# Kernel optimization log

Measured on AMD Instinct MI355X. Metric: run time of the kernel, lower is better.

## Reference

```python
import jax, jax.numpy as jnp
import numpy as np

N = 50000   # num_stocks / nodes
E = 800000  # edges (avg degree 16)
D = 64      # node_emb_dim = out_feats per head
H = 4       # num_heads
NEG_SLOPE = 0.2


def setup_inputs() -> dict:
    key = jax.random.key(0)
    ks = jax.random.split(key, 8)
    emb = jax.random.normal(ks[0], (N, D), dtype=jnp.float32)
    src = jax.random.randint(ks[1], (E,), 0, N)
    dst = jax.random.randint(ks[2], (E,), 0, N)
    W_fc = jax.random.normal(ks[3], (D, H * D), dtype=jnp.float32) * 0.05
    attn_l = jax.random.normal(ks[4], (H, D), dtype=jnp.float32) * 0.05
    attn_r = jax.random.normal(ks[5], (H, D), dtype=jnp.float32) * 0.05
    W_res = jax.random.normal(ks[6], (D, H * D), dtype=jnp.float32) * 0.05
    bias = jax.random.normal(ks[7], (H * D,), dtype=jnp.float32) * 0.05
    return {"emb": emb, "W_fc": W_fc, "attn_l": attn_l, "attn_r": attn_r,
            "W_res": W_res, "bias": bias, "src": src, "dst": dst}


def reference(emb, W_fc, attn_l, attn_r, W_res, bias, src, dst):
    n = emb.shape[0]
    # GATConv linear projection: [N, H, D]
    feat = (emb @ W_fc).reshape(n, H, D)
    # per-node attention logits: [N, H]
    el = jnp.einsum('nhd,hd->nh', feat, attn_l)
    er = jnp.einsum('nhd,hd->nh', feat, attn_r)
    # per-edge LeakyReLU attention score: [E, H]
    e = jax.nn.leaky_relu(el[src] + er[dst], negative_slope=NEG_SLOPE)
    # segmented (per-destination) softmax over incoming edges
    emax = jax.ops.segment_max(e, dst, num_segments=n)
    emax = jnp.where(jnp.isfinite(emax), emax, 0.0)  # empty segments -> -inf; make safe
    emax = jax.lax.stop_gradient(emax)               # softmax is shift-invariant
    ex = jnp.exp(e - emax[dst])                      # [E, H]
    denom = jax.ops.segment_sum(ex, dst, num_segments=n)  # [N, H]
    alpha = ex / denom[dst]                          # [E, H]
    # weighted scatter-aggregate: [N, H, D]
    rst = jax.ops.segment_sum(alpha[:, :, None] * feat[src], dst, num_segments=n)
    # residual (in_feats != H*out_feats -> linear res_fc) + bias
    resval = (emb @ W_res).reshape(n, H, D)
    rst = rst + resval + bias.reshape(1, H, D)
    # GAT.forward: mean over heads -> [N, D]
    return rst.mean(axis=1)
```

## Files before the change

kernel.cpp:

```cpp
#include <hip/hip_runtime.h>
#include <hip/hip_fp16.h>


typedef _Float16 f16x8 __attribute__((ext_vector_type(8)));
typedef _Float16 h2 __attribute__((ext_vector_type(2)));
typedef float f32x4 __attribute__((ext_vector_type(4)));

#define NGEMM 512
#define NHS   768
#define NRES  256
#define CAP   128

__device__ __forceinline__ float rflf(float v) {
    return __int_as_float(__builtin_amdgcn_readfirstlane(__float_as_int(v)));
}

__global__ __launch_bounds__(256) void k1(
    const int* __restrict__ src, const int* __restrict__ dst,
    int* __restrict__ counts, int* __restrict__ srcS, int E,
    const float* __restrict__ emb, const float* __restrict__ Wfc,
    const float* __restrict__ attnl, const float* __restrict__ attnr,
    __half* __restrict__ featH, float* __restrict__ el4, float* __restrict__ er4,
    const float* __restrict__ Wres, const float* __restrict__ bias,
    float* __restrict__ out, int N) {
    __shared__ char smem[20736];
    int tid = threadIdx.x;
    int bx = blockIdx.x;

    if (bx >= NGEMM && bx < NGEMM + NHS) {
        int base = (bx - NGEMM) * 256 + tid;
        for (int e = base; e < E; e += NHS * 256) {
            int t = dst[e];
            int s = src[e];
            int slot = atomicAdd(&counts[t], 1);
            if (slot < CAP) srcS[((size_t)t << 7) + slot] = s;
        }
        return;
    }

    if (bx >= NGEMM + NHS) {
        float* wmS = (float*)smem;
        float* bmS = (float*)(smem + 16384);
        float (*embS)[64] = (float(*)[64])(smem + 16640);
        for (int i = tid; i < 4096; i += 256) {
            int d = i >> 6, c = i & 63;
            const float* p = Wres + d * 256 + c;
            wmS[i] = 0.25f * (p[0] + p[64] + p[128] + p[192]);
        }
        if (tid < 64)
            bmS[tid] = 0.25f * (bias[tid] + bias[64 + tid] + bias[128 + tid] + bias[192 + tid]);
        __syncthreads();
        int bid = bx - NGEMM - NHS;
        int j0w = tid >> 6, lane = tid & 63;
        int ntiles = N >> 4;
        for (int tile = bid; tile < ntiles; tile += NRES) {
            int n0 = tile << 4;
            ((float4*)embS)[tid] = ((const float4*)(emb + (size_t)n0 * 64))[tid];
            __syncthreads();
            float a0 = bmS[lane], a1 = a0, a2 = a0, a3 = a0;
#pragma unroll
            for (int k = 0; k < 64; ++k) {
                float w = wmS[(k << 6) + lane];
                a0 += embS[j0w][k] * w;
                a1 += embS[j0w + 4][k] * w;
                a2 += embS[j0w + 8][k] * w;
                a3 += embS[j0w + 12][k] * w;
            }
            out[(size_t)(n0 + j0w) * 64 + lane] = a0;
            out[(size_t)(n0 + j0w + 4) * 64 + lane] = a1;
            out[(size_t)(n0 + j0w + 8) * 64 + lane] = a2;
            out[(size_t)(n0 + j0w + 12) * 64 + lane] = a3;
            __syncthreads();
        }
        return;
    }

    _Float16 (*ftH)[264] = (_Float16(*)[264])smem;
    int lane = tid & 63, w = tid >> 6;
    int lrow = lane & 15;
    int lgrp = lane >> 4;

    f16x8 bf[8];
#pragma unroll
    for (int ct = 0; ct < 4; ++ct)
#pragma unroll
        for (int kh = 0; kh < 2; ++kh) {
#pragma unroll
            for (int i = 0; i < 8; ++i) {
                int k = kh * 32 + lgrp * 8 + i;
                int c = (w << 6) + (ct << 4) + lrow;
                bf[ct * 2 + kh][i] = (_Float16)Wfc[k * 256 + c];
            }
        }
    float alr[4], arr[4];
#pragma unroll
    for (int ct = 0; ct < 4; ++ct) {
        int c = (w << 6) + (ct << 4) + lrow;
        alr[ct] = attnl[c];
        arr[ct] = attnr[c];
    }

    int ntiles = N >> 4;
    for (int tile = bx; tile < ntiles; tile += NGEMM) {
        int n0 = tile << 4;
        const float* arow = emb + (size_t)(n0 + lrow) * 64 + lgrp * 8;
        float4 a0 = *(const float4*)arow;
        float4 a1 = *(const float4*)(arow + 4);
        float4 a2 = *(const float4*)(arow + 32);
        float4 a3 = *(const float4*)(arow + 36);
        f16x8 af0, af1;
        af0[0] = (_Float16)a0.x; af0[1] = (_Float16)a0.y;
        af0[2] = (_Float16)a0.z; af0[3] = (_Float16)a0.w;
        af0[4] = (_Float16)a1.x; af0[5] = (_Float16)a1.y;
        af0[6] = (_Float16)a1.z; af0[7] = (_Float16)a1.w;
        af1[0] = (_Float16)a2.x; af1[1] = (_Float16)a2.y;
        af1[2] = (_Float16)a2.z; af1[3] = (_Float16)a2.w;
        af1[4] = (_Float16)a3.x; af1[5] = (_Float16)a3.y;
        af1[6] = (_Float16)a3.z; af1[7] = (_Float16)a3.w;

        f32x4 acc[4];
#pragma unroll
        for (int ct = 0; ct < 4; ++ct) acc[ct] = (f32x4){0.f, 0.f, 0.f, 0.f};
#pragma unroll
        for (int ct = 0; ct < 4; ++ct) {
            acc[ct] = __builtin_amdgcn_mfma_f32_16x16x32_f16(af0, bf[ct * 2 + 0], acc[ct], 0, 0, 0);
            acc[ct] = __builtin_amdgcn_mfma_f32_16x16x32_f16(af1, bf[ct * 2 + 1], acc[ct], 0, 0, 0);
        }

        float pl[4], pr[4];
#pragma unroll
        for (int i = 0; i < 4; ++i) {
            pl[i] = acc[0][i] * alr[0] + acc[1][i] * alr[1] +
                    acc[2][i] * alr[2] + acc[3][i] * alr[3];
            pr[i] = acc[0][i] * arr[0] + acc[1][i] * arr[1] +
                    acc[2][i] * arr[2] + acc[3][i] * arr[3];
        }
#pragma unroll
        for (int off = 1; off < 16; off <<= 1)
#pragma unroll
            for (int i = 0; i < 4; ++i) {
                pl[i] += __shfl_xor(pl[i], off);
                pr[i] += __shfl_xor(pr[i], off);
            }
        if (lrow == 0) {
#pragma unroll
            for (int i = 0; i < 4; ++i) {
                int n = n0 + (lgrp << 2) + i;
                el4[n * 4 + w] = pl[i];
                er4[n * 4 + w] = pr[i];
            }
        }

#pragma unroll
        for (int ct = 0; ct < 4; ++ct)
#pragma unroll
            for (int i = 0; i < 4; ++i)
                ftH[(lgrp << 2) + i][(((ct << 4) + lrow) << 2) + w] = (_Float16)acc[ct][i];
        __syncthreads();
        {
            uint4* gdst = (uint4*)(featH + (size_t)n0 * 256);
#pragma unroll
            for (int it = 0; it < 2; ++it) {
                int chunk = it * 256 + tid;
                int row = chunk >> 5, c16 = chunk & 31;
                gdst[chunk] = *(const uint4*)&ftH[row][c16 * 8];
            }
        }
        __syncthreads();
    }
}

__global__ __launch_bounds__(256) void k_agg(const int* __restrict__ counts,
                                             const int* __restrict__ srcS,
                                             const float* __restrict__ el4,
                                             const float* __restrict__ er4,
                                             const __half* __restrict__ featH,
                                             float* __restrict__ out, int N) {
    int tid = threadIdx.x;
    int lane = tid & 63;
    int nbase = blockIdx.x * 16 + ((tid >> 6) << 2);

    float base_o[4];
#pragma unroll
    for (int r = 0; r < 4; ++r)
        base_o[r] = out[(size_t)(nbase + r) * 64 + lane];

    int4 ct4 = *(const int4*)(counts + nbase);
    int cnt_[4] = {min(ct4.x, CAP), min(ct4.y, CAP), min(ct4.z, CAP), min(ct4.w, CAP)};
    int mmax = 1;
#pragma unroll
    for (int r = 0; r < 4; ++r) mmax = cnt_[r] > mmax ? cnt_[r] : mmax;

    if (mmax <= 64) {
        float4 e4_[4];
        int sj_[4];
#pragma unroll
        for (int r = 0; r < 4; ++r) {
            e4_[r] = (float4){0.f, 0.f, 0.f, 0.f};
            sj_[r] = 0;
            if (lane < cnt_[r]) sj_[r] = srcS[((size_t)(nbase + r) << 7) + lane];
        }
#pragma unroll
        for (int r = 0; r < 4; ++r) {
            if (lane < cnt_[r]) {
                float4 ern = *(const float4*)(er4 + 4 * (size_t)(nbase + r));
                float4 l = *(const float4*)(el4 + 4 * (size_t)sj_[r]);
                float x0 = l.x + ern.x, x1 = l.y + ern.y;
                float x2 = l.z + ern.z, x3 = l.w + ern.w;
                x0 = x0 > 0.f ? x0 : 0.2f * x0;
                x1 = x1 > 0.f ? x1 : 0.2f * x1;
                x2 = x2 > 0.f ? x2 : 0.2f * x2;
                x3 = x3 > 0.f ? x3 : 0.2f * x3;
                e4_[r].x = __expf(x0); e4_[r].y = __expf(x1);
                e4_[r].z = __expf(x2); e4_[r].w = __expf(x3);
            }
        }
        float4 den_[4];
#pragma unroll
        for (int r = 0; r < 4; ++r) den_[r] = e4_[r];
        for (int off = 1; off < mmax; off <<= 1) {
#pragma unroll
            for (int r = 0; r < 4; ++r) {
                den_[r].x += __shfl_xor(den_[r].x, off);
                den_[r].y += __shfl_xor(den_[r].y, off);
                den_[r].z += __shfl_xor(den_[r].z, off);
                den_[r].w += __shfl_xor(den_[r].w, off);
            }
        }
        int pk01_[4], pk23_[4];
#pragma unroll
        for (int r = 0; r < 4; ++r) {
            float ivx = 0.25f * __builtin_amdgcn_rcpf(rflf(den_[r].x));
            float ivy = 0.25f * __builtin_amdgcn_rcpf(rflf(den_[r].y));
            float ivz = 0.25f * __builtin_amdgcn_rcpf(rflf(den_[r].z));
            float ivw = 0.25f * __builtin_amdgcn_rcpf(rflf(den_[r].w));
            auto c01 = __builtin_amdgcn_cvt_pkrtz(e4_[r].x * ivx, e4_[r].y * ivy);
            auto c23 = __builtin_amdgcn_cvt_pkrtz(e4_[r].z * ivz, e4_[r].w * ivw);
            pk01_[r] = __builtin_bit_cast(int, c01);
            pk23_[r] = __builtin_bit_cast(int, c23);
        }
        float accA_[4], accB_[4], accC_[4], accD_[4];
#pragma unroll
        for (int r = 0; r < 4; ++r) { accA_[r] = accB_[r] = accC_[r] = accD_[r] = 0.f; }
        for (int j0 = 0; j0 < mmax; j0 += 4) {
            uint2 u[4][4];
#pragma unroll
            for (int r = 0; r < 4; ++r) {
                if (j0 < cnt_[r]) {
#pragma unroll
                    for (int q = 0; q < 4; ++q) {
                        int s = __builtin_amdgcn_readlane(sj_[r], j0 + q);
                        u[r][q] = *(const uint2*)(featH + ((size_t)s << 8) + (lane << 2));
                    }
                }
            }
#pragma unroll
            for (int r = 0; r < 4; ++r) {
                if (j0 < cnt_[r]) {
#pragma unroll
                    for (int q = 0; q < 4; ++q) {
                        int a01 = __builtin_amdgcn_readlane(pk01_[r], j0 + q);
                        int a23 = __builtin_amdgcn_readlane(pk23_[r], j0 + q);
                        h2 f01 = __builtin_bit_cast(h2, u[r][q].x);
                        h2 f23 = __builtin_bit_cast(h2, u[r][q].y);
                        h2 w01 = __builtin_bit_cast(h2, a01);
                        h2 w23 = __builtin_bit_cast(h2, a23);
                        if (q & 1) {
                            accC_[r] = __builtin_amdgcn_fdot2(f01, w01, accC_[r], false);
                            accD_[r] = __builtin_amdgcn_fdot2(f23, w23, accD_[r], false);
                        } else {
                            accA_[r] = __builtin_amdgcn_fdot2(f01, w01, accA_[r], false);
                            accB_[r] = __builtin_amdgcn_fdot2(f23, w23, accB_[r], false);
                        }
                    }
                }
            }
        }
#pragma unroll
        for (int r = 0; r < 4; ++r)
            out[(size_t)(nbase + r) * 64 + lane] =
                base_o[r] + ((accA_[r] + accC_[r]) + (accB_[r] + accD_[r]));
        return;
    }

    for (int r = 0; r < 4; ++r) {
        int n = nbase + r;
        int cnt = cnt_[r];
        size_t start = (size_t)n << 7;
        if (cnt == 0) { out[(size_t)n * 64 + lane] = base_o[r]; continue; }
        float4 ern = *(const float4*)(er4 + 4 * (size_t)n);
        float4 den = {0.f, 0.f, 0.f, 0.f};
        for (int i0 = 0; i0 < cnt; i0 += 64) {
            int m = min(64, cnt - i0);
            float4 e4 = {0.f, 0.f, 0.f, 0.f};
            if (lane < m) {
                int sj = srcS[start + i0 + lane];
                float4 l = *(const float4*)(el4 + 4 * (size_t)sj);
                float x0 = l.x + ern.x, x1 = l.y + ern.y;
                float x2 = l.z + ern.z, x3 = l.w + ern.w;
                x0 = x0 > 0.f ? x0 : 0.2f * x0;
                x1 = x1 > 0.f ? x1 : 0.2f * x1;
                x2 = x2 > 0.f ? x2 : 0.2f * x2;
                x3 = x3 > 0.f ? x3 : 0.2f * x3;
                e4.x = __expf(x0); e4.y = __expf(x1);
                e4.z = __expf(x2); e4.w = __expf(x3);
            }
            den.x += e4.x; den.y += e4.y; den.z += e4.z; den.w += e4.w;
        }
#pragma unroll
        for (int off = 32; off; off >>= 1) {
            den.x += __shfl_xor(den.x, off);
            den.y += __shfl_xor(den.y, off);
            den.z += __shfl_xor(den.z, off);
            den.w += __shfl_xor(den.w, off);
        }
        float ivx = 0.25f * __builtin_amdgcn_rcpf(den.x);
        float ivy = 0.25f * __builtin_amdgcn_rcpf(den.y);
        float ivz = 0.25f * __builtin_amdgcn_rcpf(den.z);
        float ivw = 0.25f * __builtin_amdgcn_rcpf(den.w);
        float accA = 0.f, accB = 0.f;
        for (int i0 = 0; i0 < cnt; i0 += 64) {
            int m = min(64, cnt - i0);
            float4 e4 = {0.f, 0.f, 0.f, 0.f};
            int sj = 0;
            if (lane < m) {
                sj = srcS[start + i0 + lane];
                float4 l = *(const float4*)(el4 + 4 * (size_t)sj);
                float x0 = l.x + ern.x, x1 = l.y + ern.y;
                float x2 = l.z + ern.z, x3 = l.w + ern.w;
                x0 = x0 > 0.f ? x0 : 0.2f * x0;
                x1 = x1 > 0.f ? x1 : 0.2f * x1;
                x2 = x2 > 0.f ? x2 : 0.2f * x2;
                x3 = x3 > 0.f ? x3 : 0.2f * x3;
                e4.x = __expf(x0); e4.y = __expf(x1);
                e4.z = __expf(x2); e4.w = __expf(x3);
            }
            auto c01 = __builtin_amdgcn_cvt_pkrtz(e4.x * ivx, e4.y * ivy);
            auto c23 = __builtin_amdgcn_cvt_pkrtz(e4.z * ivz, e4.w * ivw);
            int pk01 = __builtin_bit_cast(int, c01);
            int pk23 = __builtin_bit_cast(int, c23);
            for (int j = 0; j < m; ++j) {
                int s = __builtin_amdgcn_readlane(sj, j);
                uint2 u = *(const uint2*)(featH + ((size_t)s << 8) + (lane << 2));
                int a01 = __builtin_amdgcn_readlane(pk01, j);
                int a23 = __builtin_amdgcn_readlane(pk23, j);
                accA = __builtin_amdgcn_fdot2(__builtin_bit_cast(h2, u.x),
                                              __builtin_bit_cast(h2, a01), accA, false);
                accB = __builtin_amdgcn_fdot2(__builtin_bit_cast(h2, u.y),
                                              __builtin_bit_cast(h2, a23), accB, false);
            }
        }
        out[(size_t)n * 64 + lane] = base_o[r] + accA + accB;
    }
}

extern "C" void kernel_launch(void* const* d_in, const int* in_sizes, int n_in,
                              void* d_out, int out_size, void* d_ws, size_t ws_size,
                              hipStream_t stream) {
    const float* emb   = (const float*)d_in[0];
    const float* Wfc   = (const float*)d_in[1];
    const float* attnl = (const float*)d_in[2];
    const float* attnr = (const float*)d_in[3];
    const float* Wres  = (const float*)d_in[4];
    const float* bias  = (const float*)d_in[5];
    const int*   src   = (const int*)d_in[6];
    const int*   dst   = (const int*)d_in[7];
    int N = in_sizes[0] / 64;
    int E = in_sizes[6];
    float* out = (float*)d_out;

    __half* featH  = (__half*)d_ws;
    float*  el4    = (float*)(featH + (size_t)N * 256);
    float*  er4    = el4 + (size_t)N * 4;
    int*    counts = (int*)(er4 + (size_t)N * 4);
    int*    srcS   = counts + N;

    (void)hipMemsetAsync(counts, 0, (size_t)N * sizeof(int), stream);

    hipLaunchKernelGGL(k1, dim3(NGEMM + NHS + NRES), dim3(256), 0, stream,
                       src, dst, counts, srcS, E,
                       emb, Wfc, attnl, attnr, featH, el4, er4, Wres, bias, out, N);
    hipLaunchKernelGGL(k_agg, dim3(N / 16), dim3(256), 0, stream,
                       counts, srcS, el4, er4, featH, out, N);
}
```

Before: 203.7 us.

## Fold residual GEMM into MFMA path and merge edge bucketing into same blocks

The residual projection (head-averaged Wres and bias) now runs as an fp16 MFMA using the same A fragments already loaded for the feature GEMM, replacing the separate scalar-FMA residual blocks. Edge bucketing by destination moves from dedicated blocks into a tail loop that every one of 1024 uniform blocks runs after its GEMM tiles. This removes the heterogeneous block roles and a second read of emb. In exchange the residual is computed in fp16 rather than fp32, and the atomic bucketing no longer overlaps with GEMM work in other blocks.

```diff
diff --git a/kernel.cpp b/kernel.cpp
--- a/kernel.cpp
+++ b/kernel.cpp
@@ -6,9 +6,7 @@
 typedef _Float16 h2 __attribute__((ext_vector_type(2)));
 typedef float f32x4 __attribute__((ext_vector_type(4)));
 
-#define NGEMM 512
-#define NHS   768
-#define NRES  256
+#define NBLK1 1024
 #define CAP   128
 
 __device__ __forceinline__ float rflf(float v) {
@@ -23,59 +21,9 @@
     __half* __restrict__ featH, float* __restrict__ el4, float* __restrict__ er4,
     const float* __restrict__ Wres, const float* __restrict__ bias,
     float* __restrict__ out, int N) {
-    __shared__ char smem[20736];
+    __shared__ _Float16 ftH[16][264];
     int tid = threadIdx.x;
     int bx = blockIdx.x;
-
-    if (bx >= NGEMM && bx < NGEMM + NHS) {
-        int base = (bx - NGEMM) * 256 + tid;
-        for (int e = base; e < E; e += NHS * 256) {
-            int t = dst[e];
-            int s = src[e];
-            int slot = atomicAdd(&counts[t], 1);
-            if (slot < CAP) srcS[((size_t)t << 7) + slot] = s;
-        }
-        return;
-    }
-
-    if (bx >= NGEMM + NHS) {
-        float* wmS = (float*)smem;
-        float* bmS = (float*)(smem + 16384);
-        float (*embS)[64] = (float(*)[64])(smem + 16640);
-        for (int i = tid; i < 4096; i += 256) {
-            int d = i >> 6, c = i & 63;
-            const float* p = Wres + d * 256 + c;
-            wmS[i] = 0.25f * (p[0] + p[64] + p[128] + p[192]);
-        }
-        if (tid < 64)
-            bmS[tid] = 0.25f * (bias[tid] + bias[64 + tid] + bias[128 + tid] + bias[192 + tid]);
-        __syncthreads();
-        int bid = bx - NGEMM - NHS;
-        int j0w = tid >> 6, lane = tid & 63;
-        int ntiles = N >> 4;
-        for (int tile = bid; tile < ntiles; tile += NRES) {
-            int n0 = tile << 4;
-            ((float4*)embS)[tid] = ((const float4*)(emb + (size_t)n0 * 64))[tid];
-            __syncthreads();
-            float a0 = bmS[lane], a1 = a0, a2 = a0, a3 = a0;
-#pragma unroll
-            for (int k = 0; k < 64; ++k) {
-                float w = wmS[(k << 6) + lane];
-                a0 += embS[j0w][k] * w;
-                a1 += embS[j0w + 4][k] * w;
-                a2 += embS[j0w + 8][k] * w;
-                a3 += embS[j0w + 12][k] * w;
-            }
-            out[(size_t)(n0 + j0w) * 64 + lane] = a0;
-            out[(size_t)(n0 + j0w + 4) * 64 + lane] = a1;
-            out[(size_t)(n0 + j0w + 8) * 64 + lane] = a2;
-            out[(size_t)(n0 + j0w + 12) * 64 + lane] = a3;
-            __syncthreads();
-        }
-        return;
-    }
-
-    _Float16 (*ftH)[264] = (_Float16(*)[264])smem;
     int lane = tid & 63, w = tid >> 6;
     int lrow = lane & 15;
     int lgrp = lane >> 4;
@@ -92,6 +40,23 @@
                 bf[ct * 2 + kh][i] = (_Float16)Wfc[k * 256 + c];
             }
         }
+    f16x8 rf[2];
+    {
+        int c = (w << 4) + lrow;
+#pragma unroll
+        for (int kh = 0; kh < 2; ++kh)
+#pragma unroll
+            for (int i = 0; i < 8; ++i) {
+                int k = kh * 32 + lgrp * 8 + i;
+                const float* p = Wres + k * 256 + c;
+                rf[kh][i] = (_Float16)(0.25f * (p[0] + p[64] + p[128] + p[192]));
+            }
+    }
+    float bm;
+    {
+        int c = (w << 4) + lrow;
+        bm = 0.25f * (bias[c] + bias[64 + c] + bias[128 + c] + bias[192 + c]);
+    }
     float alr[4], arr[4];
 #pragma unroll
     for (int ct = 0; ct < 4; ++ct) {
@@ -101,7 +66,7 @@
     }
 
     int ntiles = N >> 4;
-    for (int tile = bx; tile < ntiles; tile += NGEMM) {
+    for (int tile = bx; tile < ntiles; tile += NBLK1) {
         int n0 = tile << 4;
         const float* arow = emb + (size_t)(n0 + lrow) * 64 + lgrp * 8;
         float4 a0 = *(const float4*)arow;
@@ -118,6 +83,15 @@
         af1[4] = (_Float16)a3.x; af1[5] = (_Float16)a3.y;
         af1[6] = (_Float16)a3.z; af1[7] = (_Float16)a3.w;
 
+        f32x4 accR = (f32x4){0.f, 0.f, 0.f, 0.f};
+        accR = __builtin_amdgcn_mfma_f32_16x16x32_f16(af0, rf[0], accR, 0, 0, 0);
+        accR = __builtin_amdgcn_mfma_f32_16x16x32_f16(af1, rf[1], accR, 0, 0, 0);
+#pragma unroll
+        for (int i = 0; i < 4; ++i) {
+            int n = n0 + (lgrp << 2) + i;
+            out[(size_t)n * 64 + (w << 4) + lrow] = accR[i] + bm;
+        }
+
         f32x4 acc[4];
 #pragma unroll
         for (int ct = 0; ct < 4; ++ct) acc[ct] = (f32x4){0.f, 0.f, 0.f, 0.f};
@@ -167,6 +141,13 @@
             }
         }
         __syncthreads();
+    }
+
+    for (int e = bx * 256 + tid; e < E; e += NBLK1 * 256) {
+        int t = dst[e];
+        int s = src[e];
+        int slot = atomicAdd(&counts[t], 1);
+        if (slot < CAP) srcS[((size_t)t << 7) + slot] = s;
     }
 }
 
@@ -377,7 +358,7 @@
 
     (void)hipMemsetAsync(counts, 0, (size_t)N * sizeof(int), stream);
 
-    hipLaunchKernelGGL(k1, dim3(NGEMM + NHS + NRES), dim3(256), 0, stream,
+    hipLaunchKernelGGL(k1, dim3(NBLK1), dim3(256), 0, stream,
                        src, dst, counts, srcS, E,
                        emb, Wfc, attnl, attnr, featH, el4, er4, Wres, bias, out, N);
     hipLaunchKernelGGL(k_agg, dim3(N / 16), dim3(256), 0, stream,
```

Result: slower. 215.9 us (+6.0%).
